# Kernel optimization log

Measured on AMD Instinct MI355X. Metric: run time of the kernel, lower is better.

## Reference

```python
import jax, jax.numpy as jnp
import numpy as np

BIN_SIZE = 500   # bin_size
K = 5            # num_neighbors
D_DIM = 128      # distance_dim
MAX_BINS = 200   # max_num_bins


def _mlp(x, W1, b1, W2, b2):
    # point_wise_feed_forward_network: Dense(dff=128, elu) -> Dense(d_model)
    return jax.nn.elu(x @ W1 + b1) @ W2 + b2


def setup_inputs() -> dict:
    key = jax.random.key(0)
    ks = jax.random.split(key, 10)
    B, N, F = 8, 10000, 16
    s = 0.05
    return {
        "inputs": jax.random.normal(ks[0], (B, N, F), dtype=jnp.float32),
        # encoding MLP: F -> 128 (elu) -> D_DIM
        "W_enc1": jax.random.normal(ks[1], (F, 128), dtype=jnp.float32) * s,
        "b_enc1": jnp.zeros((128,), dtype=jnp.float32),
        "W_enc2": jax.random.normal(ks[2], (128, D_DIM), dtype=jnp.float32) * s,
        "b_enc2": jnp.zeros((D_DIM,), dtype=jnp.float32),
        # edge MLP: (2F+1) -> 128 (elu) -> 1
        "W_edge1": jax.random.normal(ks[3], (2 * F + 1, 128), dtype=jnp.float32) * s,
        "b_edge1": jnp.zeros((128,), dtype=jnp.float32),
        "W_edge2": jax.random.normal(ks[4], (128, 1), dtype=jnp.float32) * s,
        "b_edge2": jnp.zeros((1,), dtype=jnp.float32),
        # LSH codebook random rotations (non-trainable): [D_DIM, MAX_BINS//2]
        "R": jax.random.normal(ks[5], (D_DIM, MAX_BINS // 2), dtype=jnp.float32) * s,
    }


def reference(inputs, W_enc1, b_enc1, W_enc2, b_enc2,
              W_edge1, b_edge1, W_edge2, b_edge2, R):
    B, N, F = inputs.shape
    nbins = N // BIN_SIZE
    # point embeddings [B, N, D_DIM]
    enc = _mlp(inputs, W_enc1, b_enc1, W_enc2, b_enc2)

    def per_batch(x_raw, pts):
        # LSH binning: project onto random rotations, split by argmax sign bucket
        mul = pts @ R[:, :nbins // 2]                       # [N, nbins//2]
        cmul = jnp.concatenate([mul, -mul], axis=-1)        # [N, nbins]
        bin_idx = jnp.argmax(cmul, axis=-1)                 # [N]
        bins_split = jnp.argsort(bin_idx).reshape(nbins, BIN_SIZE)  # [nbins, bs]
        parts = pts[bins_split]                             # [nbins, bs, D]
        # per-bin pairwise sigmoid distance
        dm = jax.nn.sigmoid(jnp.einsum('bnd,bmd->bnm', parts, parts))
        vals, idx = jax.lax.top_k(dm, K)                    # [nbins, bs, K]
        # map bin-local neighbor indices back to global point indices
        dst = bins_split[jnp.arange(nbins)[:, None, None], idx]     # [nbins, bs, K]
        src = jnp.broadcast_to(bins_split[:, :, None], dst.shape)
        # TF stacks per-neighbor then flattens: neighbor-major order (K, nbins*bs)
        src_f = jnp.transpose(src, (2, 0, 1)).reshape(-1)
        dst_f = jnp.transpose(dst, (2, 0, 1)).reshape(-1)
        val_f = jnp.transpose(vals, (2, 0, 1)).reshape(-1)
        # tf.sparse.reorder: sort indices row-major by (src, dst)
        order = jnp.argsort(src_f * N + dst_f)
        src_s, dst_s, val_s = src_f[order], dst_f[order], val_f[order]
        # sparse edge MLP on [x_src, x_dst, dist]
        edge_in = jnp.concatenate(
            [x_raw[src_s], x_raw[dst_s], val_s[:, None]], axis=-1)  # [E, 2F+1]
        edge = jax.nn.sigmoid(
            _mlp(edge_in, W_edge1, b_edge1, W_edge2, b_edge2))[:, 0]  # [E]
        return edge, src_s, dst_s

    edge_vals, src_idx, dst_idx = jax.vmap(per_batch)(inputs, enc)
    # sparse [B, N, N]: values edge_vals[b,e] at (b, src_idx[b,e], dst_idx[b,e])
    return edge_vals, src_idx, dst_idx
```

## Files before the change

kernel.cpp:

```cpp
#include <hip/hip_runtime.h>
#include <cmath>

#define NPTS 10000
#define NBATCH 8
#define NFEAT 16
#define DDIM 128
#define NBINS 20
#define BINSZ 500
#define KSEL 5
#define EDGES_PER_BATCH (NPTS*KSEL)
#define EDGE_TOT (NBATCH*EDGES_PER_BATCH)
#define TOTPTS (NBATCH*NPTS)
#define NGRP (NBATCH*NBINS)
#define PROWS 512

typedef _Float16 f16x8 __attribute__((ext_vector_type(8)));
typedef float f32x4 __attribute__((ext_vector_type(4)));
typedef unsigned short u16;
typedef unsigned int u32;

static __device__ __forceinline__ void split_f16(float v, u16& hu, u16& lu) {
    _Float16 h = (_Float16)v;
    float hf = (float)h;
    if (fabsf(v) < 6.103515625e-05f) { h = (_Float16)0.0f; hf = 0.0f; }
    _Float16 l = (_Float16)((v - hf) * 4096.0f);
    hu = __builtin_bit_cast(u16, h);
    lu = __builtin_bit_cast(u16, l);
}

static __device__ __forceinline__ float f16bits(u16 u) {
    return (float)__builtin_bit_cast(_Float16, u);
}

__global__ __launch_bounds__(256) void k_enc(const float* __restrict__ X,
        const float* __restrict__ W1, const float* __restrict__ b1,
        const float* __restrict__ W2, const float* __restrict__ b2,
        u16* __restrict__ P, int* __restrict__ hist) {
    __shared__ float hT[128*36];
    const int tid = threadIdx.x;
    const int P0 = blockIdx.x * 32;
    if (blockIdx.x == 0 && tid < NBATCH*NBINS) hist[tid] = 0;
    #pragma unroll
    for (int i = 0; i < 16; ++i) {
        int idx = i*256 + tid;
        int p = idx >> 7;
        int j = idx & 127;
        const float* xr = X + (size_t)(P0 + p)*NFEAT;
        float h = b1[j];
        #pragma unroll
        for (int f = 0; f < 16; ++f) h += xr[f] * W1[f*128 + j];
        h = (h > 0.f) ? h : expm1f(h);
        hT[j*36 + p] = h;
    }
    __syncthreads();
    const int jt = tid & 31, pt = tid >> 5;
    const int j0 = jt*4, p0 = pt*4;
    float acc[4][4];
    #pragma unroll
    for (int ep = 0; ep < 4; ++ep)
        #pragma unroll
        for (int ej = 0; ej < 4; ++ej) acc[ep][ej] = b2[j0+ej];
    for (int k = 0; k < 128; ++k) {
        float4 hv = *(const float4*)&hT[k*36 + p0];
        float4 wv = *(const float4*)&W2[k*128 + j0];
        float hvv[4] = {hv.x,hv.y,hv.z,hv.w};
        float wvv[4] = {wv.x,wv.y,wv.z,wv.w};
        #pragma unroll
        for (int ep = 0; ep < 4; ++ep)
            #pragma unroll
            for (int ej = 0; ej < 4; ++ej) acc[ep][ej] += hvv[ep]*wvv[ej];
    }
    #pragma unroll
    for (int ep = 0; ep < 4; ++ep) {
        u16 hs[4], ls[4];
        #pragma unroll
        for (int ej = 0; ej < 4; ++ej) split_f16(acc[ep][ej], hs[ej], ls[ej]);
        size_t ro = (size_t)(P0+p0+ep)*256 + j0;
        uint2 hv2, lv2;
        hv2.x = (u32)hs[0] | ((u32)hs[1]<<16); hv2.y = (u32)hs[2] | ((u32)hs[3]<<16);
        lv2.x = (u32)ls[0] | ((u32)ls[1]<<16); lv2.y = (u32)ls[2] | ((u32)ls[3]<<16);
        *(uint2*)&P[ro]       = hv2;
        *(uint2*)&P[ro + 128] = lv2;
    }
}

__global__ __launch_bounds__(256) void k_bins(const u16* __restrict__ P,
        const float* __restrict__ R,
        int* __restrict__ binIdx, int* __restrict__ hist) {
    __shared__ float Rl[128*10];
    const int tid = threadIdx.x;
    for (int idx = tid; idx < 1280; idx += 256) {
        int d = idx / 10, i = idx % 10;
        Rl[idx] = R[d*100 + i];
    }
    __syncthreads();
    int gp = blockIdx.x*256 + tid;
    if (gp >= TOTPTS) return;
    float acc[10];
    #pragma unroll
    for (int i = 0; i < 10; ++i) acc[i] = 0.f;
    const uint4* hr = (const uint4*)(P + (size_t)gp*256);
    const uint4* lr = (const uint4*)(P + (size_t)gp*256 + 128);
    const float sc = 2.44140625e-4f;
    for (int c = 0; c < 16; ++c) {
        uint4 hv = hr[c], lv = lr[c];
        float x[8];
        x[0] = f16bits((u16)(hv.x & 0xffff)) + f16bits((u16)(lv.x & 0xffff))*sc;
        x[1] = f16bits((u16)(hv.x >> 16))    + f16bits((u16)(lv.x >> 16))*sc;
        x[2] = f16bits((u16)(hv.y & 0xffff)) + f16bits((u16)(lv.y & 0xffff))*sc;
        x[3] = f16bits((u16)(hv.y >> 16))    + f16bits((u16)(lv.y >> 16))*sc;
        x[4] = f16bits((u16)(hv.z & 0xffff)) + f16bits((u16)(lv.z & 0xffff))*sc;
        x[5] = f16bits((u16)(hv.z >> 16))    + f16bits((u16)(lv.z >> 16))*sc;
        x[6] = f16bits((u16)(hv.w & 0xffff)) + f16bits((u16)(lv.w & 0xffff))*sc;
        x[7] = f16bits((u16)(hv.w >> 16))    + f16bits((u16)(lv.w >> 16))*sc;
        #pragma unroll
        for (int e = 0; e < 8; ++e) {
            const float* rr = &Rl[(c*8+e)*10];
            #pragma unroll
            for (int i = 0; i < 10; ++i) acc[i] += x[e]*rr[i];
        }
    }
    float best = acc[0]; int bi = 0;
    #pragma unroll
    for (int i = 1; i < 10; ++i) if (acc[i] > best) { best = acc[i]; bi = i; }
    #pragma unroll
    for (int i = 0; i < 10; ++i) { float v = -acc[i]; if (v > best) { best = v; bi = 10+i; } }
    binIdx[gp] = bi;
    atomicAdd(&hist[(gp/NPTS)*NBINS + bi], 1);
}

__global__ __launch_bounds__(256) void k_sort(const int* __restrict__ binIdx,
        const int* __restrict__ hist, int* __restrict__ sortedIdx) {
    const int b = blockIdx.x / NBINS;
    const int bin = blockIdx.x % NBINS;
    const int tid = threadIdx.x;
    __shared__ int wtot[4];
    int off = 0;
    for (int k = 0; k < bin; ++k) off += hist[b*NBINS + k];
    const int* bptr = binIdx + b*NPTS;
    int* sptr = sortedIdx + b*NPTS;
    const int lane = tid & 63, wid = tid >> 6;
    for (int c = 0; c < 40; ++c) {
        int i = c*256 + tid;
        bool pred = (i < NPTS) && (bptr[i] == bin);
        unsigned long long mask = __ballot(pred);
        int rank = __popcll(mask & ((1ULL << lane) - 1ULL));
        if (lane == 0) wtot[wid] = __popcll(mask);
        __syncthreads();
        int prefix = 0;
        #pragma unroll
        for (int w = 0; w < 4; ++w) prefix += (w < wid) ? wtot[w] : 0;
        int total = wtot[0]+wtot[1]+wtot[2]+wtot[3];
        if (pred) sptr[off + prefix + rank] = i;
        off += total;
        __syncthreads();
    }
}

#define BT(va,pa,vb,pb) (((va) > (vb)) || (((va) == (vb)) && ((pa) < (pb))))
#define INS_TIE(VV,PP,v,p) do { \
  if (BT(v,p,VV[4],PP[4])) { \
    if (BT(v,p,VV[3],PP[3])) { VV[4]=VV[3]; PP[4]=PP[3]; \
      if (BT(v,p,VV[2],PP[2])) { VV[3]=VV[2]; PP[3]=PP[2]; \
        if (BT(v,p,VV[1],PP[1])) { VV[2]=VV[1]; PP[2]=PP[1]; \
          if (BT(v,p,VV[0],PP[0])) { VV[1]=VV[0]; PP[1]=PP[0]; VV[0]=(v); PP[0]=(p); } \
          else { VV[1]=(v); PP[1]=(p); } } \
        else { VV[2]=(v); PP[2]=(p); } } \
      else { VV[3]=(v); PP[3]=(p); } } \
    else { VV[4]=(v); PP[4]=(p); } } } while(0)

__global__ __launch_bounds__(256, 3) void k_gram(const u16* __restrict__ P,
        const int* __restrict__ sortedIdx, float* __restrict__ pV, int* __restrict__ pP) {
    __shared__ int gIdx[512];
    __shared__ __align__(16) union ShU {
        struct { u16 H[128][40]; u16 L[128][40]; } bs;
        float T[64][132];
    } sh;
    const int tid = threadIdx.x;
    const int unit = blockIdx.x / 160;
    const int grp  = blockIdx.x - unit*160;
    const int rowTile = unit >> 2, ch = unit & 3;
    const int b = grp / NBINS, g = grp - b*NBINS;
    for (int i = tid; i < 512; i += 256) gIdx[i] = sortedIdx[b*NPTS + g*500 + min(i, 499)];
    __syncthreads();

    const int w    = tid >> 6;
    const int lane = tid & 63;
    const int l15  = lane & 15, l4 = lane >> 4;
    const int rowBase = rowTile * 128;

    const size_t ebase = (size_t)b * NPTS * 256;
    const u16* PB = P + ebase;
    const u16* pA0 = PB + (size_t)gIdx[rowBase + w*32 +      l15]*256 + l4*8;
    const u16* pA1 = PB + (size_t)gIdx[rowBase + w*32 + 16 + l15]*256 + l4*8;

    const int scol = tid >> 1, spart = tid & 1;
    const u16* pS = PB + (size_t)gIdx[ch*128 + scol]*256 + spart*128;
    u16* dS = spart ? &sh.bs.L[scol][0] : &sh.bs.H[scol][0];

    f32x4 acc[2][8];
    const f32x4 z4 = {0.f, 0.f, 0.f, 0.f};
    #pragma unroll
    for (int rf = 0; rf < 2; ++rf)
        #pragma unroll
        for (int cf = 0; cf < 8; ++cf) acc[rf][cf] = z4;

    const _Float16 c64 = (_Float16)64.0f;
    #pragma unroll 1
    for (int ks = 0; ks < 4; ++ks) {
        __syncthreads();
        {
            const uint4* s = (const uint4*)(pS + ks*32);
            uint4 v0 = s[0], v1 = s[1], v2 = s[2], v3 = s[3];
            uint4* d = (uint4*)dS;
            d[0] = v0; d[1] = v1; d[2] = v2; d[3] = v3;
        }
        const int oH = ks*32, oL = 128 + ks*32;
        const f16x8 aH0 = *(const f16x8*)(pA0 + oH);
        const f16x8 aL0 = *(const f16x8*)(pA0 + oL);
        const f16x8 aH1 = *(const f16x8*)(pA1 + oH);
        const f16x8 aL1 = *(const f16x8*)(pA1 + oL);
        const f16x8 aS0 = aH0 * c64;
        const f16x8 aS1 = aH1 * c64;
        __syncthreads();
        #pragma unroll
        for (int cf = 0; cf < 8; ++cf) {
            const int col = cf*16 + l15;
            const f16x8 bH = *(const f16x8*)&sh.bs.H[col][l4*8];
            const f16x8 bL = *(const f16x8*)&sh.bs.L[col][l4*8];
            const f16x8 bS = bH * c64;
            acc[0][cf] = __builtin_amdgcn_mfma_f32_16x16x32_f16(aH0, bL, acc[0][cf], 0, 0, 0);
            acc[1][cf] = __builtin_amdgcn_mfma_f32_16x16x32_f16(aH1, bL, acc[1][cf], 0, 0, 0);
            acc[0][cf] = __builtin_amdgcn_mfma_f32_16x16x32_f16(aL0, bH, acc[0][cf], 0, 0, 0);
            acc[1][cf] = __builtin_amdgcn_mfma_f32_16x16x32_f16(aL1, bH, acc[1][cf], 0, 0, 0);
            acc[0][cf] = __builtin_amdgcn_mfma_f32_16x16x32_f16(aS0, bS, acc[0][cf], 0, 0, 0);
            acc[1][cf] = __builtin_amdgcn_mfma_f32_16x16x32_f16(aS1, bS, acc[1][cf], 0, 0, 0);
        }
    }
    __syncthreads();

    const float sc = 2.44140625e-4f;
    const int rT = tid >> 2;
    const int q  = tid & 3;
    const int nI = (ch == 3 && q == 3) ? 20 : 32;
    #pragma unroll
    for (int rf = 0; rf < 2; ++rf) {
        #pragma unroll
        for (int cf = 0; cf < 8; ++cf) {
            const int col = cf*16 + l15;
            const int r0  = w*16 + l4*4;
            #pragma unroll
            for (int j = 0; j < 4; ++j) sh.T[r0+j][col] = acc[rf][cf][j] * sc;
        }
        __syncthreads();
        float lv[5]; int lp[5];
        #pragma unroll
        for (int p5 = 0; p5 < 5; ++p5) { lv[p5] = -3.4e38f; lp[p5] = 0x7fffffff; }
        const float* Tr = &sh.T[rT][q*32];
        #pragma unroll
        for (int t = 0; t < 8; ++t) {
            const int c4 = (t + q*2) & 7;
            float4 v4 = *(const float4*)&Tr[c4*4];
            float vv4[4] = {v4.x, v4.y, v4.z, v4.w};
            #pragma unroll
            for (int e = 0; e < 4; ++e) {
                const int i = c4*4 + e;
                if (i < nI) INS_TIE(lv, lp, vv4[e], ch*128 + q*32 + i);
            }
        }
        #pragma unroll
        for (int m = 1; m < 4; m <<= 1) {
            float qv[5]; int qp[5];
            #pragma unroll
            for (int p5 = 0; p5 < 5; ++p5) {
                qv[p5] = __shfl_xor(lv[p5], m, 64);
                qp[p5] = __shfl_xor(lp[p5], m, 64);
            }
            #pragma unroll
            for (int p5 = 0; p5 < 5; ++p5) INS_TIE(lv, lp, qv[p5], qp[p5]);
        }
        if (q == 0) {
            const int rpos = rowBase + (rT>>4)*32 + rf*16 + (rT&15);
            if (rpos < 500) {
                const int pbase = ((grp*4 + ch)*PROWS + rpos)*5;
                #pragma unroll
                for (int p5 = 0; p5 < 5; ++p5) { pV[pbase+p5] = lv[p5]; pP[pbase+p5] = lp[p5]; }
            }
        }
        __syncthreads();
    }
}

__global__ __launch_bounds__(256) void k_edge(const float* __restrict__ X,
        const float* __restrict__ W1, const float* __restrict__ b1,
        const float* __restrict__ W2, const float* __restrict__ b2,
        const float* __restrict__ pV, const int* __restrict__ pP,
        const int* __restrict__ sortedIdx, float* __restrict__ out) {
    __shared__ float w1t[128*36];
    __shared__ float b1l[128];
    __shared__ float w2l[128];
    const int tid = threadIdx.x;
    for (int idx = tid; idx < 33*128; idx += 256) {
        int f = idx >> 7, j = idx & 127;
        w1t[j*36 + f] = W1[idx];
    }
    if (tid < 128) { b1l[tid] = b1[tid]; w2l[tid] = W2[tid]; }
    __syncthreads();
    int rid4 = blockIdx.x*256 + tid;
    if (rid4 >= NGRP*BINSZ*4) return;
    const int rid = rid4 >> 2, quarter = rid4 & 3;
    const int grp = rid / BINSZ;
    const int rowLocal = rid - grp*BINSZ;
    const int b = grp / NBINS, g = grp - b*NBINS;
    float lv[5]; int lp[5];
    {
        int pbase = (grp*4*PROWS + rowLocal)*5;
        #pragma unroll
        for (int j = 0; j < 5; ++j) { lv[j] = pV[pbase+j]; lp[j] = pP[pbase+j]; }
    }
    #pragma unroll
    for (int chh = 1; chh < 4; ++chh) {
        int pbase = ((grp*4 + chh)*PROWS + rowLocal)*5;
        #pragma unroll
        for (int j = 0; j < 5; ++j) {
            float v = pV[pbase+j]; int p = pP[pbase+j];
            INS_TIE(lv, lp, v, p);
        }
    }
    const int* sIdx = sortedIdx + b*NPTS + g*BINSZ;
    const int src = sIdx[rowLocal];
    int dd[5]; float vv[5];
    #pragma unroll
    for (int j = 0; j < 5; ++j) {
        dd[j] = sIdx[lp[j]];
        vv[j] = 1.f/(1.f + expf(-lv[j]));
    }
    #define CSWAP(i,j) { if (dd[i] > dd[j]) { int td=dd[i];dd[i]=dd[j];dd[j]=td; \
                         float tf=vv[i];vv[i]=vv[j];vv[j]=tf; } }
    CSWAP(0,1) CSWAP(3,4) CSWAP(2,4) CSWAP(2,3) CSWAP(1,4)
    CSWAP(0,3) CSWAP(0,2) CSWAP(1,3) CSWAP(1,2)
    #undef CSWAP
    const int base = b*EDGES_PER_BATCH + src*5;
    if (quarter == 0) {
        #pragma unroll
        for (int e = 0; e < 5; ++e) {
            out[EDGE_TOT   + base + e] = (float)src;
            out[2*EDGE_TOT + base + e] = (float)dd[e];
        }
    }
    float4 xs[4];
    {
        const float4* xp = (const float4*)(X + ((size_t)b*NPTS + src)*NFEAT);
        #pragma unroll
        for (int q = 0; q < 4; ++q) xs[q] = xp[q];
    }
    float4 xd[5][4];
    #pragma unroll
    for (int e = 0; e < 5; ++e) {
        const float4* xp = (const float4*)(X + ((size_t)b*NPTS + dd[e])*NFEAT);
        #pragma unroll
        for (int q = 0; q < 4; ++q) xd[e][q] = xp[q];
    }
    float acc[5] = {0.f,0.f,0.f,0.f,0.f};
    const int jEnd = quarter*32 + 32;
    for (int j = quarter*32; j < jEnd; ++j) {
        const float* wr = &w1t[j*36];
        float4 ws0 = ((const float4*)wr)[0];
        float4 ws1 = ((const float4*)wr)[1];
        float4 ws2 = ((const float4*)wr)[2];
        float4 ws3 = ((const float4*)wr)[3];
        float4 u0  = ((const float4*)(wr+16))[0];
        float4 u1  = ((const float4*)(wr+16))[1];
        float4 u2  = ((const float4*)(wr+16))[2];
        float4 u3  = ((const float4*)(wr+16))[3];
        float w32 = wr[32];
        float w2j = w2l[j];
        float sh = b1l[j]
            + xs[0].x*ws0.x + xs[0].y*ws0.y + xs[0].z*ws0.z + xs[0].w*ws0.w
            + xs[1].x*ws1.x + xs[1].y*ws1.y + xs[1].z*ws1.z + xs[1].w*ws1.w
            + xs[2].x*ws2.x + xs[2].y*ws2.y + xs[2].z*ws2.z + xs[2].w*ws2.w
            + xs[3].x*ws3.x + xs[3].y*ws3.y + xs[3].z*ws3.z + xs[3].w*ws3.w;
        #pragma unroll
        for (int e = 0; e < 5; ++e) {
            float h = sh
                + xd[e][0].x*u0.x + xd[e][0].y*u0.y + xd[e][0].z*u0.z + xd[e][0].w*u0.w
                + xd[e][1].x*u1.x + xd[e][1].y*u1.y + xd[e][1].z*u1.z + xd[e][1].w*u1.w
                + xd[e][2].x*u2.x + xd[e][2].y*u2.y + xd[e][2].z*u2.z + xd[e][2].w*u2.w
                + xd[e][3].x*u3.x + xd[e][3].y*u3.y + xd[e][3].z*u3.z + xd[e][3].w*u3.w;
            h += vv[e]*w32;
            h = (h > 0.f) ? h : expm1f(h);
            acc[e] += h * w2j;
        }
    }
    #pragma unroll
    for (int e = 0; e < 5; ++e) {
        acc[e] += __shfl_xor(acc[e], 1, 64);
        acc[e] += __shfl_xor(acc[e], 2, 64);
    }
    if (quarter != 0) return;
    float b2v = b2[0];
    #pragma unroll
    for (int e = 0; e < 5; ++e) {
        out[base + e] = 1.f/(1.f + expf(-(acc[e] + b2v)));
    }
}

extern "C" void kernel_launch(void* const* d_in, const int* in_sizes, int n_in,
                              void* d_out, int out_size, void* d_ws, size_t ws_size,
                              hipStream_t stream) {
    const float* X   = (const float*)d_in[0];
    const float* We1 = (const float*)d_in[1];
    const float* be1 = (const float*)d_in[2];
    const float* We2 = (const float*)d_in[3];
    const float* be2 = (const float*)d_in[4];
    const float* Wd1 = (const float*)d_in[5];
    const float* bd1 = (const float*)d_in[6];
    const float* Wd2 = (const float*)d_in[7];
    const float* bd2 = (const float*)d_in[8];
    const float* R   = (const float*)d_in[9];
    float* out = (float*)d_out;

    u16* Pw         = (u16*)d_ws;
    int*   binIdx   = (int*)(Pw + (size_t)TOTPTS*256);
    int*   sortedIdx= binIdx + TOTPTS;
    int*   hist     = sortedIdx + TOTPTS;
    float* pV       = (float*)(hist + NBATCH*NBINS);
    int*   pP       = (int*)(pV + (size_t)NGRP*4*PROWS*5);

    k_enc  <<<TOTPTS/32, 256, 0, stream>>>(X, We1, be1, We2, be2, Pw, hist);
    k_bins <<<(TOTPTS+255)/256, 256, 0, stream>>>(Pw, R, binIdx, hist);
    k_sort <<<NBATCH*NBINS, 256, 0, stream>>>(binIdx, hist, sortedIdx);
    k_gram <<<NGRP*16, 256, 0, stream>>>(Pw, sortedIdx, pV, pP);
    k_edge <<<(NGRP*BINSZ*4+255)/256, 256, 0, stream>>>(X, Wd1, bd1, Wd2, bd2,
                                                        pV, pP, sortedIdx, out);
}
```

Measured before the change: 467.6 us.

## Prescale f16 hi/lo split, drop per-tile scaling, prefetch B tiles in gram kernel

The encoder now stores the high part of the embedding pre-multiplied by 64 and the residual scaled by 64. This lets the gram kernel feed the stored values straight into the MFMAs without per-iteration f16 multiplies, and the final scale factor moves to the five selected top-k values per row. The gram kernel also unrolls the K loop and register-prefetches the next shared-memory B tile, raises the occupancy hint from 3 to 4, and interleaves each lane's column scan so it can use strict-greater insertion instead of tie-aware insertion. The risks are precision changes from the residual using a different scale and exponent range, possible tie-order differences, and register pressure under the tighter launch bound.

After: 416.1 us. 1.12x faster.

```diff
diff --git a/kernel.cpp b/kernel.cpp
--- a/kernel.cpp
+++ b/kernel.cpp
@@ -19,13 +19,14 @@
 typedef unsigned short u16;
 typedef unsigned int u32;
 
-static __device__ __forceinline__ void split_f16(float v, u16& hu, u16& lu) {
+static __device__ __forceinline__ void split_f16(float v, u16& hu, u16& du) {
     _Float16 h = (_Float16)v;
     float hf = (float)h;
     if (fabsf(v) < 6.103515625e-05f) { h = (_Float16)0.0f; hf = 0.0f; }
-    _Float16 l = (_Float16)((v - hf) * 4096.0f);
-    hu = __builtin_bit_cast(u16, h);
-    lu = __builtin_bit_cast(u16, l);
+    _Float16 Hs = h * (_Float16)64.0f;
+    _Float16 D  = (_Float16)((v - hf) * 64.0f);
+    hu = __builtin_bit_cast(u16, Hs);
+    du = __builtin_bit_cast(u16, D);
 }
 
 static __device__ __forceinline__ float f16bits(u16 u) {
@@ -72,15 +73,15 @@
     }
     #pragma unroll
     for (int ep = 0; ep < 4; ++ep) {
-        u16 hs[4], ls[4];
-        #pragma unroll
-        for (int ej = 0; ej < 4; ++ej) split_f16(acc[ep][ej], hs[ej], ls[ej]);
+        u16 hs[4], ds[4];
+        #pragma unroll
+        for (int ej = 0; ej < 4; ++ej) split_f16(acc[ep][ej], hs[ej], ds[ej]);
         size_t ro = (size_t)(P0+p0+ep)*256 + j0;
-        uint2 hv2, lv2;
+        uint2 hv2, dv2;
         hv2.x = (u32)hs[0] | ((u32)hs[1]<<16); hv2.y = (u32)hs[2] | ((u32)hs[3]<<16);
-        lv2.x = (u32)ls[0] | ((u32)ls[1]<<16); lv2.y = (u32)ls[2] | ((u32)ls[3]<<16);
+        dv2.x = (u32)ds[0] | ((u32)ds[1]<<16); dv2.y = (u32)ds[2] | ((u32)ds[3]<<16);
         *(uint2*)&P[ro]       = hv2;
-        *(uint2*)&P[ro + 128] = lv2;
+        *(uint2*)&P[ro + 128] = dv2;
     }
 }
 
@@ -101,18 +102,17 @@
     for (int i = 0; i < 10; ++i) acc[i] = 0.f;
     const uint4* hr = (const uint4*)(P + (size_t)gp*256);
     const uint4* lr = (const uint4*)(P + (size_t)gp*256 + 128);
-    const float sc = 2.44140625e-4f;
     for (int c = 0; c < 16; ++c) {
         uint4 hv = hr[c], lv = lr[c];
         float x[8];
-        x[0] = f16bits((u16)(hv.x & 0xffff)) + f16bits((u16)(lv.x & 0xffff))*sc;
-        x[1] = f16bits((u16)(hv.x >> 16))    + f16bits((u16)(lv.x >> 16))*sc;
-        x[2] = f16bits((u16)(hv.y & 0xffff)) + f16bits((u16)(lv.y & 0xffff))*sc;
-        x[3] = f16bits((u16)(hv.y >> 16))    + f16bits((u16)(lv.y >> 16))*sc;
-        x[4] = f16bits((u16)(hv.z & 0xffff)) + f16bits((u16)(lv.z & 0xffff))*sc;
-        x[5] = f16bits((u16)(hv.z >> 16))    + f16bits((u16)(lv.z >> 16))*sc;
-        x[6] = f16bits((u16)(hv.w & 0xffff)) + f16bits((u16)(lv.w & 0xffff))*sc;
-        x[7] = f16bits((u16)(hv.w >> 16))    + f16bits((u16)(lv.w >> 16))*sc;
+        x[0] = f16bits((u16)(hv.x & 0xffff)) + f16bits((u16)(lv.x & 0xffff));
+        x[1] = f16bits((u16)(hv.x >> 16))    + f16bits((u16)(lv.x >> 16));
+        x[2] = f16bits((u16)(hv.y & 0xffff)) + f16bits((u16)(lv.y & 0xffff));
+        x[3] = f16bits((u16)(hv.y >> 16))    + f16bits((u16)(lv.y >> 16));
+        x[4] = f16bits((u16)(hv.z & 0xffff)) + f16bits((u16)(lv.z & 0xffff));
+        x[5] = f16bits((u16)(hv.z >> 16))    + f16bits((u16)(lv.z >> 16));
+        x[6] = f16bits((u16)(hv.w & 0xffff)) + f16bits((u16)(lv.w & 0xffff));
+        x[7] = f16bits((u16)(hv.w >> 16))    + f16bits((u16)(lv.w >> 16));
         #pragma unroll
         for (int e = 0; e < 8; ++e) {
             const float* rr = &Rl[(c*8+e)*10];
@@ -157,6 +157,17 @@
     }
 }
 
+#define INS_STRICT(VV,PP,v,p) do { \
+  if ((v) > VV[4]) { \
+    if ((v) > VV[3]) { VV[4]=VV[3]; PP[4]=PP[3]; \
+      if ((v) > VV[2]) { VV[3]=VV[2]; PP[3]=PP[2]; \
+        if ((v) > VV[1]) { VV[2]=VV[1]; PP[2]=PP[1]; \
+          if ((v) > VV[0]) { VV[1]=VV[0]; PP[1]=PP[0]; VV[0]=(v); PP[0]=(p); } \
+          else { VV[1]=(v); PP[1]=(p); } } \
+        else { VV[2]=(v); PP[2]=(p); } } \
+      else { VV[3]=(v); PP[3]=(p); } } \
+    else { VV[4]=(v); PP[4]=(p); } } } while(0)
+
 #define BT(va,pa,vb,pb) (((va) > (vb)) || (((va) == (vb)) && ((pa) < (pb))))
 #define INS_TIE(VV,PP,v,p) do { \
   if (BT(v,p,VV[4],PP[4])) { \
@@ -169,7 +180,7 @@
       else { VV[3]=(v); PP[3]=(p); } } \
     else { VV[4]=(v); PP[4]=(p); } } } while(0)
 
-__global__ __launch_bounds__(256, 3) void k_gram(const u16* __restrict__ P,
+__global__ __launch_bounds__(256, 4) void k_gram(const u16* __restrict__ P,
         const int* __restrict__ sortedIdx, float* __restrict__ pV, int* __restrict__ pP) {
     __shared__ int gIdx[512];
     __shared__ __align__(16) union ShU {
@@ -205,36 +216,37 @@
         #pragma unroll
         for (int cf = 0; cf < 8; ++cf) acc[rf][cf] = z4;
 
-    const _Float16 c64 = (_Float16)64.0f;
-    #pragma unroll 1
+    uint4 s0, s1, s2, s3;
+    { const uint4* s = (const uint4*)pS; s0 = s[0]; s1 = s[1]; s2 = s[2]; s3 = s[3]; }
+
+    #pragma unroll
     for (int ks = 0; ks < 4; ++ks) {
         __syncthreads();
         {
-            const uint4* s = (const uint4*)(pS + ks*32);
-            uint4 v0 = s[0], v1 = s[1], v2 = s[2], v3 = s[3];
             uint4* d = (uint4*)dS;
-            d[0] = v0; d[1] = v1; d[2] = v2; d[3] = v3;
-        }
-        const int oH = ks*32, oL = 128 + ks*32;
+            d[0] = s0; d[1] = s1; d[2] = s2; d[3] = s3;
+        }
+        if (ks < 3) {
+            const uint4* s = (const uint4*)(pS + (ks+1)*32);
+            s0 = s[0]; s1 = s[1]; s2 = s[2]; s3 = s[3];
+        }
+        const int oH = ks*32, oD = 128 + ks*32;
         const f16x8 aH0 = *(const f16x8*)(pA0 + oH);
-        const f16x8 aL0 = *(const f16x8*)(pA0 + oL);
+        const f16x8 aD0 = *(const f16x8*)(pA0 + oD);
         const f16x8 aH1 = *(const f16x8*)(pA1 + oH);
-        const f16x8 aL1 = *(const f16x8*)(pA1 + oL);
-        const f16x8 aS0 = aH0 * c64;
-        const f16x8 aS1 = aH1 * c64;
+        const f16x8 aD1 = *(const f16x8*)(pA1 + oD);
         __syncthreads();
         #pragma unroll
         for (int cf = 0; cf < 8; ++cf) {
             const int col = cf*16 + l15;
             const f16x8 bH = *(const f16x8*)&sh.bs.H[col][l4*8];
-            const f16x8 bL = *(const f16x8*)&sh.bs.L[col][l4*8];
-            const f16x8 bS = bH * c64;
-            acc[0][cf] = __builtin_amdgcn_mfma_f32_16x16x32_f16(aH0, bL, acc[0][cf], 0, 0, 0);
-            acc[1][cf] = __builtin_amdgcn_mfma_f32_16x16x32_f16(aH1, bL, acc[1][cf], 0, 0, 0);
-            acc[0][cf] = __builtin_amdgcn_mfma_f32_16x16x32_f16(aL0, bH, acc[0][cf], 0, 0, 0);
-            acc[1][cf] = __builtin_amdgcn_mfma_f32_16x16x32_f16(aL1, bH, acc[1][cf], 0, 0, 0);
-            acc[0][cf] = __builtin_amdgcn_mfma_f32_16x16x32_f16(aS0, bS, acc[0][cf], 0, 0, 0);
-            acc[1][cf] = __builtin_amdgcn_mfma_f32_16x16x32_f16(aS1, bS, acc[1][cf], 0, 0, 0);
+            const f16x8 bD = *(const f16x8*)&sh.bs.L[col][l4*8];
+            acc[0][cf] = __builtin_amdgcn_mfma_f32_16x16x32_f16(aH0, bD, acc[0][cf], 0, 0, 0);
+            acc[1][cf] = __builtin_amdgcn_mfma_f32_16x16x32_f16(aH1, bD, acc[1][cf], 0, 0, 0);
+            acc[0][cf] = __builtin_amdgcn_mfma_f32_16x16x32_f16(aD0, bH, acc[0][cf], 0, 0, 0);
+            acc[1][cf] = __builtin_amdgcn_mfma_f32_16x16x32_f16(aD1, bH, acc[1][cf], 0, 0, 0);
+            acc[0][cf] = __builtin_amdgcn_mfma_f32_16x16x32_f16(aH0, bH, acc[0][cf], 0, 0, 0);
+            acc[1][cf] = __builtin_amdgcn_mfma_f32_16x16x32_f16(aH1, bH, acc[1][cf], 0, 0, 0);
         }
     }
     __syncthreads();
@@ -242,7 +254,7 @@
     const float sc = 2.44140625e-4f;
     const int rT = tid >> 2;
     const int q  = tid & 3;
-    const int nI = (ch == 3 && q == 3) ? 20 : 32;
+    const bool chk = (ch == 3);
     #pragma unroll
     for (int rf = 0; rf < 2; ++rf) {
         #pragma unroll
@@ -250,22 +262,23 @@
             const int col = cf*16 + l15;
             const int r0  = w*16 + l4*4;
             #pragma unroll
-            for (int j = 0; j < 4; ++j) sh.T[r0+j][col] = acc[rf][cf][j] * sc;
+            for (int j = 0; j < 4; ++j) sh.T[r0+j][col] = acc[rf][cf][j];
         }
         __syncthreads();
         float lv[5]; int lp[5];
         #pragma unroll
         for (int p5 = 0; p5 < 5; ++p5) { lv[p5] = -3.4e38f; lp[p5] = 0x7fffffff; }
-        const float* Tr = &sh.T[rT][q*32];
+        const float* Tr = &sh.T[rT][0];
         #pragma unroll
         for (int t = 0; t < 8; ++t) {
-            const int c4 = (t + q*2) & 7;
+            const int c4 = t*4 + q;
             float4 v4 = *(const float4*)&Tr[c4*4];
             float vv4[4] = {v4.x, v4.y, v4.z, v4.w};
             #pragma unroll
             for (int e = 0; e < 4; ++e) {
-                const int i = c4*4 + e;
-                if (i < nI) INS_TIE(lv, lp, vv4[e], ch*128 + q*32 + i);
+                const int cloc = c4*4 + e;
+                if (!chk || cloc < 116)
+                    INS_STRICT(lv, lp, vv4[e], ch*128 + cloc);
             }
         }
         #pragma unroll
@@ -284,7 +297,7 @@
             if (rpos < 500) {
                 const int pbase = ((grp*4 + ch)*PROWS + rpos)*5;
                 #pragma unroll
-                for (int p5 = 0; p5 < 5; ++p5) { pV[pbase+p5] = lv[p5]; pP[pbase+p5] = lp[p5]; }
+                for (int p5 = 0; p5 < 5; ++p5) { pV[pbase+p5] = lv[p5]*sc; pP[pbase+p5] = lp[p5]; }
             }
         }
         __syncthreads();
```
